# Kernel optimization log

Hardware: AMD Instinct MI355X
Metric: run time of the kernel (lower is better)

The kernel has to match this reference:

```python
import jax, jax.numpy as jnp
import numpy as np

NUM_HEADS = 8
MAX_REL = 32  # max_relative_positions
LN_EPS = 1e-5


def _conv1x1(x, W, b):
    # x: (B, C, H, W), W: (Cout, Cin), b: (Cout,)
    return jnp.einsum('bchw,oc->bohw', x, W) + b[None, :, None, None]


def setup_inputs() -> dict:
    key = jax.random.key(0)
    ks = jax.random.split(key, 10)
    B, C, H, W = 2, 512, 48, 48
    L = H * W
    s = 1.0 / np.sqrt(C)
    inp = {
        'x': jax.random.normal(ks[0], (B, C, H, W), jnp.float32),
        'mask': jax.random.randint(ks[1], (1, NUM_HEADS, L, L), 0, 2).astype(bool),
        'learnable_pos': jax.random.normal(ks[2], (1, C, H, W), jnp.float32) * 0.02,
        'Wq': jax.random.normal(ks[3], (C, C), jnp.float32) * s,
        'bq': jnp.zeros((C,), jnp.float32),
        'Wk': jax.random.normal(ks[4], (C, C), jnp.float32) * s,
        'bk': jnp.zeros((C,), jnp.float32),
        'Wv': jax.random.normal(ks[5], (C, C), jnp.float32) * s,
        'bv': jnp.zeros((C,), jnp.float32),
        'Wo': jax.random.normal(ks[6], (C, C), jnp.float32) * s,
        'bo': jnp.zeros((C,), jnp.float32),
        'rel_table': jax.random.normal(ks[7], (NUM_HEADS, 2 * MAX_REL + 1), jnp.float32) * 0.02,
        'ln_gamma': jnp.ones((C,), jnp.float32),
        'ln_beta': jnp.zeros((C,), jnp.float32),
    }
    return inp


def reference(x, mask, learnable_pos, Wq, bq, Wk, bk, Wv, bv, Wo, bo,
              rel_table, ln_gamma, ln_beta):
    B, C, H, W = x.shape
    L = H * W
    hd = C // NUM_HEADS
    residual = x

    xp = x + learnable_pos
    q = _conv1x1(xp, Wq, bq)
    k = _conv1x1(xp, Wk, bk)
    v = _conv1x1(xp, Wv, bv)

    def split_heads(t):  # (B,C,H,W) -> (B, heads, L, hd)
        return t.reshape(B, NUM_HEADS, hd, L).transpose(0, 1, 3, 2)

    q, k, v = split_heads(q), split_heads(k), split_heads(v)

    scale = 1.0 / np.sqrt(hd).astype(np.float32)
    scores = jnp.einsum('bhld,bhmd->bhlm', q, k) * scale  # (B,H,L,L)

    # relative positional bias per head
    pos = jnp.arange(L)
    rp = jnp.clip(pos[:, None] - pos[None, :], -MAX_REL, MAX_REL) + MAX_REL  # (L,L)
    scores = scores + rel_table[:, rp][None]  # (1,heads,L,L) broadcast

    scores = jnp.where(mask, scores, jnp.float32(-1e9))
    attn = jax.nn.softmax(scores, axis=-1)

    out = jnp.einsum('bhlm,bhmd->bhld', attn, v)  # (B,heads,L,hd)
    out = out.transpose(0, 1, 3, 2).reshape(B, C, H, W)
    out = _conv1x1(out, Wo, bo)

    y = residual + out
    # LayerNorm over channels (channels-last permute in original)
    yl = y.transpose(0, 2, 3, 1)  # (B,H,W,C)
    mu = jnp.mean(yl, axis=-1, keepdims=True)
    var = jnp.var(yl, axis=-1, keepdims=True)
    yl = (yl - mu) * jax.lax.rsqrt(var + LN_EPS) * ln_gamma + ln_beta
    return yl.transpose(0, 3, 1, 2)
```

## Files before the change

kernel.cpp:

```cpp
#include <hip/hip_runtime.h>
#include <cstdint>

#define L_SEQ 2304
#define CDIM  512
#define NHEADS 8
#define HD    64
#define LL    ((size_t)L_SEQ * L_SEQ)
#define ROWS_TOT (16 * L_SEQ)
#define PERBL ((size_t)2 * L_SEQ * 512)

typedef short  s8v  __attribute__((ext_vector_type(8)));
typedef float  f4v  __attribute__((ext_vector_type(4)));

__device__ __forceinline__ ushort f2bf(float f) {
    union { float f; uint32_t u; } v; v.f = f;
    uint32_t u = v.u;
    uint32_t r = (u + 0x7FFFu + ((u >> 16) & 1u)) >> 16;
    return (ushort)r;
}

__device__ __forceinline__ float bf2f(ushort u) {
    union { uint32_t u; float f; } v; v.u = (uint32_t)u << 16;
    return v.f;
}

__global__ __launch_bounds__(256) void prep_w(
    const float* __restrict__ Wq, const float* __restrict__ Wk,
    const float* __restrict__ Wv, const float* __restrict__ Wo,
    ushort* __restrict__ wf)
{
    const int i    = blockIdx.x * 256 + threadIdx.x;
    const int lane = i & 63;
    const int F    = (i >> 6) & 63;
    const int ob   = (i >> 12) & 7;
    const int mat  = i >> 15;
    const float* src = (mat == 0) ? Wq : (mat == 1) ? Wk : (mat == 2) ? Wv : Wo;
    const int row = ob * 64 + (F & 3) * 16 + (lane & 15);
    const int col = (F >> 2) * 32 + (lane >> 4) * 8;
    const float4 w0 = *(const float4*)&src[(size_t)row * 512 + col];
    const float4 w1 = *(const float4*)&src[(size_t)row * 512 + col + 4];
    ushort4 o0, o1;
    o0.x = f2bf(w0.x); o0.y = f2bf(w0.y); o0.z = f2bf(w0.z); o0.w = f2bf(w0.w);
    o1.x = f2bf(w1.x); o1.y = f2bf(w1.y); o1.z = f2bf(w1.z); o1.w = f2bf(w1.w);
    *(ushort4*)&wf[(size_t)i * 8]     = o0;
    *(ushort4*)&wf[(size_t)i * 8 + 4] = o1;
}

__global__ __launch_bounds__(256) void xpose(
    const float* __restrict__ x, const float* __restrict__ pos,
    ushort* __restrict__ xt)
{
    __shared__ ushort T[64][72];
    const int l0 = blockIdx.x * 64;
    const int c0 = blockIdx.y * 64;
    const int b  = blockIdx.z;
    const int t  = threadIdx.x;
    const int cc = t >> 2;
    const int l4 = (t & 3) * 16;
    const size_t off  = ((size_t)b * CDIM + c0 + cc) * L_SEQ + l0 + l4;
    const size_t poff = (size_t)(c0 + cc) * L_SEQ + l0 + l4;
    #pragma unroll
    for (int j4 = 0; j4 < 4; j4++) {
        const float4 xv = *(const float4*)&x[off + j4 * 4];
        const float4 pv = *(const float4*)&pos[poff + j4 * 4];
        T[cc][l4 + j4 * 4 + 0] = f2bf(xv.x + pv.x);
        T[cc][l4 + j4 * 4 + 1] = f2bf(xv.y + pv.y);
        T[cc][l4 + j4 * 4 + 2] = f2bf(xv.z + pv.z);
        T[cc][l4 + j4 * 4 + 3] = f2bf(xv.w + pv.w);
    }
    __syncthreads();
    const int lr = t >> 2;
    const int c4 = (t & 3) * 16;
    ushort o[16];
    #pragma unroll
    for (int j = 0; j < 16; j++) o[j] = T[c4 + j][lr];
    ushort* dst = &xt[((size_t)b * L_SEQ + l0 + lr) * 512 + c0 + c4];
    *(ushort4*)&dst[0]  = *(ushort4*)&o[0];
    *(ushort4*)&dst[4]  = *(ushort4*)&o[4];
    *(ushort4*)&dst[8]  = *(ushort4*)&o[8];
    *(ushort4*)&dst[12] = *(ushort4*)&o[12];
}

__global__ __launch_bounds__(256) void qkv_mfma(
    const ushort* __restrict__ xt, const ushort* __restrict__ wf,
    const float* __restrict__ bq, const float* __restrict__ bk,
    const float* __restrict__ bv,
    ushort* __restrict__ q_t, ushort* __restrict__ k_t, ushort* __restrict__ v_t)
{
    const int l0 = blockIdx.x * 64;
    const int ob = blockIdx.y;
    const int o0 = ob * 64;
    const int b  = blockIdx.z;
    const int t = threadIdx.x, w = t >> 6, lane = t & 63;
    const int n16 = lane & 15, q4 = lane >> 4;

    const ushort* A = xt + ((size_t)b * L_SEQ + l0 + w * 16 + n16) * 512 + q4 * 8;

    s8v areg[16];
    #pragma unroll
    for (int i = 0; i < 16; i++) areg[i] = *(const s8v*)&A[i * 32];

    const size_t lb = (size_t)lane * 8;

    f4v acc[3][4] = {};
    for (int ks = 0; ks < 16; ks++) {
        s8v bf[3][4];
        #pragma unroll
        for (int m = 0; m < 3; m++)
            #pragma unroll
            for (int t4 = 0; t4 < 4; t4++)
                bf[m][t4] = *(const s8v*)&wf[
                    ((size_t)((m * 8 + ob) * 64 + ks * 4 + t4)) * 512 + lb];
        const s8v a = areg[ks];
        #pragma unroll
        for (int m = 0; m < 3; m++)
            #pragma unroll
            for (int t4 = 0; t4 < 4; t4++)
                acc[m][t4] = __builtin_amdgcn_mfma_f32_16x16x32_bf16(a, bf[m][t4], acc[m][t4], 0, 0, 0);
    }

    const int h = ob;
    const int rowbase = l0 + w * 16 + q4 * 4;

    #pragma unroll
    for (int m = 0; m < 2; m++) {
        const float* bias = (m == 0) ? bq : bk;
        const float sc = (m == 0) ? 0.125f : 1.0f;
        ushort* op = (m == 0 ? q_t : k_t) + ((size_t)(b * NHEADS + h)) * L_SEQ * HD;
        #pragma unroll
        for (int t4 = 0; t4 < 4; t4++) {
            const float bi = bias[o0 + t4 * 16 + n16];
            #pragma unroll
            for (int r = 0; r < 4; r++)
                op[(size_t)(rowbase + r) * HD + t4 * 16 + n16] = f2bf((acc[m][t4][r] + bi) * sc);
        }
    }
    {
        ushort* op = v_t + ((size_t)(b * NHEADS + h)) * HD * L_SEQ;
        #pragma unroll
        for (int t4 = 0; t4 < 4; t4++) {
            const float bi = bv[o0 + t4 * 16 + n16];
            ushort4 st;
            st.x = f2bf(acc[2][t4][0] + bi);
            st.y = f2bf(acc[2][t4][1] + bi);
            st.z = f2bf(acc[2][t4][2] + bi);
            st.w = f2bf(acc[2][t4][3] + bi);
            *(ushort4*)&op[(size_t)(t4 * 16 + n16) * L_SEQ + rowbase] = st;
        }
    }
}

__global__ __launch_bounds__(256) void flash_attn_mfma(
    const ushort* __restrict__ q, const ushort* __restrict__ k,
    const ushort* __restrict__ vt, const int* __restrict__ mask,
    const float* __restrict__ rel_table, ushort* __restrict__ Opart,
    float* __restrict__ Lpart)
{
    __shared__ __align__(16) ushort Kf[512 * 8];
    __shared__ __align__(16) ushort Vf[512 * 8];
    __shared__ __align__(16) ushort Pb[4 * 16 * 72];
    __shared__ float rt[65];

    const int t    = threadIdx.x;
    const int id   = blockIdx.x;
    const int h    = id & 7;
    const int s2   = id >> 3;
    const int b    = s2 & 1;
    const int half = (s2 >> 1) & 1;
    const int qb   = s2 >> 2;
    const int bh   = b * NHEADS + h;
    const int l0   = qb * 64;
    const int w    = t >> 6;
    const int lane = t & 63;
    const int n16  = lane & 15;
    const int q4   = lane >> 4;

    if (t < 65) rt[t] = rel_table[h * 65 + t];

    const ushort* qp = q  + (size_t)bh * L_SEQ * HD;
    const ushort* kp = k  + (size_t)bh * L_SEQ * HD;
    const ushort* vp = vt + (size_t)bh * HD * L_SEQ;
    const int*    mp = mask + (size_t)h * LL;

    const int qrow = l0 + w * 16 + n16;
    const s8v qA0 = *(const s8v*)&qp[(size_t)qrow * HD + q4 * 8];
    const s8v qA1 = *(const s8v*)&qp[(size_t)qrow * HD + 32 + q4 * 8];

    f4v O[4] = {{0.f,0.f,0.f,0.f},{0.f,0.f,0.f,0.f},{0.f,0.f,0.f,0.f},{0.f,0.f,0.f,0.f}};
    float lrun[4] = {0.f, 0.f, 0.f, 0.f};

    int sKey[2], sD0[2], sDd[2];
    #pragma unroll
    for (int cc = 0; cc < 2; cc++) {
        const int c = t + cc * 256;
        const int g = c >> 6;
        const int sT = g >> 1, sS = g & 1;
        const int sQ = (c >> 4) & 3, sN = c & 15;
        sKey[cc] = sT * 16 + sN;
        sD0[cc]  = sS * 32 + sQ * 8;
        sDd[cc]  = sT * 16 + sN;
    }

    const int rowbase = l0 + w * 16 + q4 * 4;
    const int kbase = half * 1152;

    s8v kreg[2], vreg[2];
    int mreg[4][4];
    #pragma unroll
    for (int cc = 0; cc < 2; cc++) {
        kreg[cc] = *(const s8v*)&kp[(size_t)(kbase + sKey[cc]) * HD + sD0[cc]];
        vreg[cc] = *(const s8v*)&vp[(size_t)sDd[cc] * L_SEQ + kbase + sD0[cc]];
    }
    #pragma unroll
    for (int t4 = 0; t4 < 4; t4++)
        #pragma unroll
        for (int r = 0; r < 4; r++)
            mreg[t4][r] = mp[(size_t)(rowbase + r) * L_SEQ + kbase + t4 * 16 + n16];

    for (int mt = 0; mt < 18; mt++) {
        const int mb = kbase + mt * 64;
        __syncthreads();
        #pragma unroll
        for (int cc = 0; cc < 2; cc++) {
            const int c = t + cc * 256;
            *(s8v*)&Kf[c * 8] = kreg[cc];
            *(s8v*)&Vf[c * 8] = vreg[cc];
        }
        __syncthreads();

        const int mb2 = (mt < 17) ? mb + 64 : mb;
        s8v knx[2], vnx[2];
        int mnx[4][4];
        #pragma unroll
        for (int cc = 0; cc < 2; cc++) {
            knx[cc] = *(const s8v*)&kp[(size_t)(mb2 + sKey[cc]) * HD + sD0[cc]];
            vnx[cc] = *(const s8v*)&vp[(size_t)sDd[cc] * L_SEQ + mb2 + sD0[cc]];
        }
        #pragma unroll
        for (int t4 = 0; t4 < 4; t4++)
            #pragma unroll
            for (int r = 0; r < 4; r++)
                mnx[t4][r] = mp[(size_t)(rowbase + r) * L_SEQ + mb2 + t4 * 16 + n16];

        f4v S[4];
        #pragma unroll
        for (int t4 = 0; t4 < 4; t4++) {
            const s8v b0 = *(const s8v*)&Kf[((t4 * 2 + 0) * 64 + lane) * 8];
            const s8v b1 = *(const s8v*)&Kf[((t4 * 2 + 1) * 64 + lane) * 8];
            f4v acc = {0.f, 0.f, 0.f, 0.f};
            acc = __builtin_amdgcn_mfma_f32_16x16x32_bf16(qA0, b0, acc, 0, 0, 0);
            acc = __builtin_amdgcn_mfma_f32_16x16x32_bf16(qA1, b1, acc, 0, 0, 0);
            S[t4] = acc;
        }

        #pragma unroll
        for (int t4 = 0; t4 < 4; t4++) {
            const int A = (l0 + w * 16) - (mb + t4 * 16);
            if (A >= 47) {
                const float bu = rt[64];
                #pragma unroll
                for (int r = 0; r < 4; r++) S[t4][r] += bu;
            } else if (A <= -47) {
                const float bu = rt[0];
                #pragma unroll
                for (int r = 0; r < 4; r++) S[t4][r] += bu;
            } else {
                #pragma unroll
                for (int r = 0; r < 4; r++) {
                    int dix = A + q4 * 4 + r - n16;
                    dix = min(max(dix, -32), 32) + 32;
                    S[t4][r] += rt[dix];
                }
            }
            #pragma unroll
            for (int r = 0; r < 4; r++)
                if (mreg[t4][r] == 0) S[t4][r] = -1e9f;
        }

        float sum[4] = {0.f, 0.f, 0.f, 0.f};
        #pragma unroll
        for (int r = 0; r < 4; r++) {
            #pragma unroll
            for (int t4 = 0; t4 < 4; t4++) {
                const float p = __expf(S[t4][r]);
                sum[r] += p;
                Pb[w * 1152 + (q4 * 4 + r) * 72 + t4 * 16 + n16] = f2bf(p);
            }
        }

        const s8v pf0 = *(const s8v*)&Pb[w * 1152 + n16 * 72 + q4 * 8];
        const s8v pf1 = *(const s8v*)&Pb[w * 1152 + n16 * 72 + 32 + q4 * 8];
        #pragma unroll
        for (int t4 = 0; t4 < 4; t4++) {
            f4v o = O[t4];
            const s8v v0 = *(const s8v*)&Vf[((t4 * 2 + 0) * 64 + lane) * 8];
            const s8v v1 = *(const s8v*)&Vf[((t4 * 2 + 1) * 64 + lane) * 8];
            o = __builtin_amdgcn_mfma_f32_16x16x32_bf16(pf0, v0, o, 0, 0, 0);
            o = __builtin_amdgcn_mfma_f32_16x16x32_bf16(pf1, v1, o, 0, 0, 0);
            O[t4] = o;
        }

        #pragma unroll
        for (int r = 0; r < 4; r++) {
            float s = sum[r];
            s += __shfl_xor(s, 1);
            s += __shfl_xor(s, 2);
            s += __shfl_xor(s, 4);
            s += __shfl_xor(s, 8);
            lrun[r] += s;
        }

        #pragma unroll
        for (int cc = 0; cc < 2; cc++) { kreg[cc] = knx[cc]; vreg[cc] = vnx[cc]; }
        #pragma unroll
        for (int t4 = 0; t4 < 4; t4++)
            #pragma unroll
            for (int r = 0; r < 4; r++)
                mreg[t4][r] = mnx[t4][r];
    }

    ushort* op = Opart + (size_t)half * PERBL + (size_t)b * L_SEQ * 512;
    #pragma unroll
    for (int r = 0; r < 4; r++) {
        const size_t base = (size_t)(rowbase + r) * 512 + h * 64;
        #pragma unroll
        for (int t4 = 0; t4 < 4; t4++)
            op[base + t4 * 16 + n16] = f2bf(O[t4][r]);
    }
    if (n16 == 0) {
        const size_t sb = (size_t)half * ROWS_TOT + (size_t)bh * L_SEQ;
        #pragma unroll
        for (int r = 0; r < 4; r++)
            Lpart[sb + rowbase + r] = lrun[r];
    }
}

__global__ __launch_bounds__(256) void combine_kernel(
    const ushort* __restrict__ O01, const float* __restrict__ Lp,
    ushort* __restrict__ at)
{
    const int i   = blockIdx.x * 256 + threadIdx.x;
    const int c8  = i & 63;
    const int row = i >> 6;
    const int b   = row / L_SEQ;
    const int l   = row - b * L_SEQ;
    const int h   = c8 >> 3;
    const size_t s = (size_t)(b * NHEADS + h) * L_SEQ + l;
    const float f = 1.0f / (Lp[s] + Lp[ROWS_TOT + s]);
    const size_t o = (size_t)row * 512 + c8 * 8;
    const ushort4 a0 = *(const ushort4*)&O01[o];
    const ushort4 a1 = *(const ushort4*)&O01[o + 4];
    const ushort4 c0 = *(const ushort4*)&O01[PERBL + o];
    const ushort4 c1 = *(const ushort4*)&O01[PERBL + o + 4];
    ushort4 r0, r1;
    r0.x = f2bf((bf2f(a0.x) + bf2f(c0.x)) * f);
    r0.y = f2bf((bf2f(a0.y) + bf2f(c0.y)) * f);
    r0.z = f2bf((bf2f(a0.z) + bf2f(c0.z)) * f);
    r0.w = f2bf((bf2f(a0.w) + bf2f(c0.w)) * f);
    r1.x = f2bf((bf2f(a1.x) + bf2f(c1.x)) * f);
    r1.y = f2bf((bf2f(a1.y) + bf2f(c1.y)) * f);
    r1.z = f2bf((bf2f(a1.z) + bf2f(c1.z)) * f);
    r1.w = f2bf((bf2f(a1.w) + bf2f(c1.w)) * f);
    *(ushort4*)&at[o]     = r0;
    *(ushort4*)&at[o + 4] = r1;
}

__global__ __launch_bounds__(256) void out_mfma(
    const ushort* __restrict__ at, const ushort* __restrict__ wf,
    const float* __restrict__ bo, const float* __restrict__ x,
    float* __restrict__ y)
{
    const int l0 = blockIdx.x * 64;
    const int ob = blockIdx.y;
    const int o0 = ob * 64;
    const int b  = blockIdx.z;
    const int t = threadIdx.x, w = t >> 6, lane = t & 63;
    const int n16 = lane & 15, q4 = lane >> 4;

    const ushort* A = at + ((size_t)b * L_SEQ + l0 + w * 16 + n16) * 512 + q4 * 8;

    s8v areg[16];
    #pragma unroll
    for (int i = 0; i < 16; i++) areg[i] = *(const s8v*)&A[i * 32];

    const size_t lb = (size_t)lane * 8;

    f4v acc[4] = {{0.f,0.f,0.f,0.f},{0.f,0.f,0.f,0.f},{0.f,0.f,0.f,0.f},{0.f,0.f,0.f,0.f}};
    for (int ks = 0; ks < 16; ks++) {
        s8v bf[4];
        #pragma unroll
        for (int t4 = 0; t4 < 4; t4++)
            bf[t4] = *(const s8v*)&wf[
                ((size_t)((3 * 8 + ob) * 64 + ks * 4 + t4)) * 512 + lb];
        const s8v a = areg[ks];
        #pragma unroll
        for (int t4 = 0; t4 < 4; t4++)
            acc[t4] = __builtin_amdgcn_mfma_f32_16x16x32_bf16(a, bf[t4], acc[t4], 0, 0, 0);
    }

    const int rowbase = l0 + w * 16 + q4 * 4;
    #pragma unroll
    for (int t4 = 0; t4 < 4; t4++) {
        const int o = o0 + t4 * 16 + n16;
        const float bi = bo[o];
        const size_t off = ((size_t)b * CDIM + o) * L_SEQ + rowbase;
        const float4 xv = *(const float4*)&x[off];
        float4 st;
        st.x = acc[t4][0] + bi + xv.x;
        st.y = acc[t4][1] + bi + xv.y;
        st.z = acc[t4][2] + bi + xv.z;
        st.w = acc[t4][3] + bi + xv.w;
        *(float4*)&y[off] = st;
    }
}

__global__ __launch_bounds__(256) void ln_kernel(
    float* __restrict__ y, const float* __restrict__ gamma,
    const float* __restrict__ beta)
{
    const int t = threadIdx.x;
    const int p = t & 31;
    const int g = t >> 5;
    const int pos = blockIdx.x * 32 + p;
    const int b = (pos >= L_SEQ) ? 1 : 0;
    const int l = pos - b * L_SEQ;
    float* col = y + (size_t)b * CDIM * L_SEQ + l;

    float s = 0.f, sq = 0.f;
    for (int c = g * 64; c < g * 64 + 64; c++) {
        const float v = col[(size_t)c * L_SEQ];
        s += v; sq += v * v;
    }
    __shared__ float S1[8][32];
    __shared__ float S2[8][32];
    S1[g][p] = s; S2[g][p] = sq;
    __syncthreads();
    if (t < 32) {
        float ss = 0.f, qq = 0.f;
        #pragma unroll
        for (int gg = 0; gg < 8; gg++) { ss += S1[gg][t]; qq += S2[gg][t]; }
        const float mu = ss * (1.0f / CDIM);
        const float var = qq * (1.0f / CDIM) - mu * mu;
        S1[0][t] = mu;
        S2[0][t] = rsqrtf(var + 1e-5f);
    }
    __syncthreads();
    const float mu = S1[0][p];
    const float rs = S2[0][p];
    for (int c = g * 64; c < g * 64 + 64; c++) {
        const float v = col[(size_t)c * L_SEQ];
        col[(size_t)c * L_SEQ] = (v - mu) * rs * gamma[c] + beta[c];
    }
}

extern "C" void kernel_launch(void* const* d_in, const int* in_sizes, int n_in,
                              void* d_out, int out_size, void* d_ws, size_t ws_size,
                              hipStream_t stream) {
    const float* x    = (const float*)d_in[0];
    const int* mask   = (const int*)d_in[1];
    const float* pos  = (const float*)d_in[2];
    const float* Wq   = (const float*)d_in[3];
    const float* bq   = (const float*)d_in[4];
    const float* Wk   = (const float*)d_in[5];
    const float* bk   = (const float*)d_in[6];
    const float* Wv   = (const float*)d_in[7];
    const float* bv   = (const float*)d_in[8];
    const float* Wo   = (const float*)d_in[9];
    const float* bo   = (const float*)d_in[10];
    const float* rel  = (const float*)d_in[11];
    const float* gam  = (const float*)d_in[12];
    const float* bet  = (const float*)d_in[13];

    ushort* qw  = (ushort*)d_ws;
    ushort* kw  = qw + PERBL;
    ushort* vw  = kw + PERBL;
    ushort* xtw = vw + PERBL;
    ushort* wbw = xtw + PERBL;
    ushort* Opart = wbw + (size_t)4 * 262144;
    float* Lpart = (float*)(Opart + 2 * PERBL);
    ushort* attnT = xtw;
    float* y = (float*)d_out;

    prep_w<<<dim3(512), 256, 0, stream>>>(Wq, Wk, Wv, Wo, wbw);

    xpose<<<dim3(L_SEQ / 64, CDIM / 64, 2), 256, 0, stream>>>(x, pos, xtw);

    qkv_mfma<<<dim3(L_SEQ / 64, CDIM / 64, 2), 256, 0, stream>>>(
        xtw, wbw, bq, bk, bv, qw, kw, vw);

    flash_attn_mfma<<<dim3(1152), 256, 0, stream>>>(qw, kw, vw, mask, rel,
                                                    Opart, Lpart);

    combine_kernel<<<dim3(1152), 256, 0, stream>>>(Opart, Lpart, attnT);

    out_mfma<<<dim3(L_SEQ / 64, CDIM / 64, 2), 256, 0, stream>>>(
        attnT, wbw, bo, x, y);

    ln_kernel<<<(2 * L_SEQ) / 32, 256, 0, stream>>>(y, gam, bet);
}
```

Before: 366.6 us.

## Fuse prep kernels, fold split-K combine into output GEMM, double-buffer K/V LDS

Merges weight conversion and input transpose into one launch, removes the separate combine kernel by normalizing and summing the two partial attention outputs while loading A-fragments in the output projection, and double-buffers K/V tiles in shared memory in the flash attention loop to drop one barrier per iteration. This cuts kernel launches and an intermediate round-trip through memory. In exchange the output GEMM reads twice as much partial data per block (repeated across output-channel blocks), and the extra LDS may lower attention occupancy.

```diff
diff --git a/kernel.cpp b/kernel.cpp
--- a/kernel.cpp
+++ b/kernel.cpp
@@ -24,61 +24,61 @@
     return v.f;
 }
 
-__global__ __launch_bounds__(256) void prep_w(
+__global__ __launch_bounds__(256) void prep(
     const float* __restrict__ Wq, const float* __restrict__ Wk,
     const float* __restrict__ Wv, const float* __restrict__ Wo,
-    ushort* __restrict__ wf)
-{
-    const int i    = blockIdx.x * 256 + threadIdx.x;
-    const int lane = i & 63;
-    const int F    = (i >> 6) & 63;
-    const int ob   = (i >> 12) & 7;
-    const int mat  = i >> 15;
-    const float* src = (mat == 0) ? Wq : (mat == 1) ? Wk : (mat == 2) ? Wv : Wo;
-    const int row = ob * 64 + (F & 3) * 16 + (lane & 15);
-    const int col = (F >> 2) * 32 + (lane >> 4) * 8;
-    const float4 w0 = *(const float4*)&src[(size_t)row * 512 + col];
-    const float4 w1 = *(const float4*)&src[(size_t)row * 512 + col + 4];
-    ushort4 o0, o1;
-    o0.x = f2bf(w0.x); o0.y = f2bf(w0.y); o0.z = f2bf(w0.z); o0.w = f2bf(w0.w);
-    o1.x = f2bf(w1.x); o1.y = f2bf(w1.y); o1.z = f2bf(w1.z); o1.w = f2bf(w1.w);
-    *(ushort4*)&wf[(size_t)i * 8]     = o0;
-    *(ushort4*)&wf[(size_t)i * 8 + 4] = o1;
-}
-
-__global__ __launch_bounds__(256) void xpose(
     const float* __restrict__ x, const float* __restrict__ pos,
-    ushort* __restrict__ xt)
+    ushort* __restrict__ wf, ushort* __restrict__ xt)
 {
     __shared__ ushort T[64][72];
-    const int l0 = blockIdx.x * 64;
-    const int c0 = blockIdx.y * 64;
-    const int b  = blockIdx.z;
+    const int bx = blockIdx.x;
     const int t  = threadIdx.x;
-    const int cc = t >> 2;
-    const int l4 = (t & 3) * 16;
-    const size_t off  = ((size_t)b * CDIM + c0 + cc) * L_SEQ + l0 + l4;
-    const size_t poff = (size_t)(c0 + cc) * L_SEQ + l0 + l4;
-    #pragma unroll
-    for (int j4 = 0; j4 < 4; j4++) {
-        const float4 xv = *(const float4*)&x[off + j4 * 4];
-        const float4 pv = *(const float4*)&pos[poff + j4 * 4];
-        T[cc][l4 + j4 * 4 + 0] = f2bf(xv.x + pv.x);
-        T[cc][l4 + j4 * 4 + 1] = f2bf(xv.y + pv.y);
-        T[cc][l4 + j4 * 4 + 2] = f2bf(xv.z + pv.z);
-        T[cc][l4 + j4 * 4 + 3] = f2bf(xv.w + pv.w);
-    }
-    __syncthreads();
-    const int lr = t >> 2;
-    const int c4 = (t & 3) * 16;
-    ushort o[16];
-    #pragma unroll
-    for (int j = 0; j < 16; j++) o[j] = T[c4 + j][lr];
-    ushort* dst = &xt[((size_t)b * L_SEQ + l0 + lr) * 512 + c0 + c4];
-    *(ushort4*)&dst[0]  = *(ushort4*)&o[0];
-    *(ushort4*)&dst[4]  = *(ushort4*)&o[4];
-    *(ushort4*)&dst[8]  = *(ushort4*)&o[8];
-    *(ushort4*)&dst[12] = *(ushort4*)&o[12];
+    if (bx < 512) {
+        const int i    = bx * 256 + t;
+        const int lane = i & 63;
+        const int F    = (i >> 6) & 63;
+        const int ob   = (i >> 12) & 7;
+        const int mat  = i >> 15;
+        const float* src = (mat == 0) ? Wq : (mat == 1) ? Wk : (mat == 2) ? Wv : Wo;
+        const int row = ob * 64 + (F & 3) * 16 + (lane & 15);
+        const int col = (F >> 2) * 32 + (lane >> 4) * 8;
+        const float4 w0 = *(const float4*)&src[(size_t)row * 512 + col];
+        const float4 w1 = *(const float4*)&src[(size_t)row * 512 + col + 4];
+        ushort4 o0, o1;
+        o0.x = f2bf(w0.x); o0.y = f2bf(w0.y); o0.z = f2bf(w0.z); o0.w = f2bf(w0.w);
+        o1.x = f2bf(w1.x); o1.y = f2bf(w1.y); o1.z = f2bf(w1.z); o1.w = f2bf(w1.w);
+        *(ushort4*)&wf[(size_t)i * 8]     = o0;
+        *(ushort4*)&wf[(size_t)i * 8 + 4] = o1;
+    } else {
+        const int bb = bx - 512;
+        const int l0 = (bb % 36) * 64;
+        const int c0 = ((bb / 36) & 7) * 64;
+        const int b  = bb / 288;
+        const int cc = t >> 2;
+        const int l4 = (t & 3) * 16;
+        const size_t off  = ((size_t)b * CDIM + c0 + cc) * L_SEQ + l0 + l4;
+        const size_t poff = (size_t)(c0 + cc) * L_SEQ + l0 + l4;
+        #pragma unroll
+        for (int j4 = 0; j4 < 4; j4++) {
+            const float4 xv = *(const float4*)&x[off + j4 * 4];
+            const float4 pv = *(const float4*)&pos[poff + j4 * 4];
+            T[cc][l4 + j4 * 4 + 0] = f2bf(xv.x + pv.x);
+            T[cc][l4 + j4 * 4 + 1] = f2bf(xv.y + pv.y);
+            T[cc][l4 + j4 * 4 + 2] = f2bf(xv.z + pv.z);
+            T[cc][l4 + j4 * 4 + 3] = f2bf(xv.w + pv.w);
+        }
+        __syncthreads();
+        const int lr = t >> 2;
+        const int c4 = (t & 3) * 16;
+        ushort o[16];
+        #pragma unroll
+        for (int j = 0; j < 16; j++) o[j] = T[c4 + j][lr];
+        ushort* dst = &xt[((size_t)b * L_SEQ + l0 + lr) * 512 + c0 + c4];
+        *(ushort4*)&dst[0]  = *(ushort4*)&o[0];
+        *(ushort4*)&dst[4]  = *(ushort4*)&o[4];
+        *(ushort4*)&dst[8]  = *(ushort4*)&o[8];
+        *(ushort4*)&dst[12] = *(ushort4*)&o[12];
+    }
 }
 
 __global__ __launch_bounds__(256) void qkv_mfma(
@@ -156,8 +156,8 @@
     const float* __restrict__ rel_table, ushort* __restrict__ Opart,
     float* __restrict__ Lpart)
 {
-    __shared__ __align__(16) ushort Kf[512 * 8];
-    __shared__ __align__(16) ushort Vf[512 * 8];
+    __shared__ __align__(16) ushort Kf[2][512 * 8];
+    __shared__ __align__(16) ushort Vf[2][512 * 8];
     __shared__ __align__(16) ushort Pb[4 * 16 * 72];
     __shared__ float rt[65];
 
@@ -217,14 +217,16 @@
         for (int r = 0; r < 4; r++)
             mreg[t4][r] = mp[(size_t)(rowbase + r) * L_SEQ + kbase + t4 * 16 + n16];
 
+    int par = 0;
     for (int mt = 0; mt < 18; mt++) {
         const int mb = kbase + mt * 64;
-        __syncthreads();
+        ushort* Kb = &Kf[par][0];
+        ushort* Vb = &Vf[par][0];
         #pragma unroll
         for (int cc = 0; cc < 2; cc++) {
             const int c = t + cc * 256;
-            *(s8v*)&Kf[c * 8] = kreg[cc];
-            *(s8v*)&Vf[c * 8] = vreg[cc];
+            *(s8v*)&Kb[c * 8] = kreg[cc];
+            *(s8v*)&Vb[c * 8] = vreg[cc];
         }
         __syncthreads();
 
@@ -245,8 +247,8 @@
         f4v S[4];
         #pragma unroll
         for (int t4 = 0; t4 < 4; t4++) {
-            const s8v b0 = *(const s8v*)&Kf[((t4 * 2 + 0) * 64 + lane) * 8];
-            const s8v b1 = *(const s8v*)&Kf[((t4 * 2 + 1) * 64 + lane) * 8];
+            const s8v b0 = *(const s8v*)&Kb[((t4 * 2 + 0) * 64 + lane) * 8];
+            const s8v b1 = *(const s8v*)&Kb[((t4 * 2 + 1) * 64 + lane) * 8];
             f4v acc = {0.f, 0.f, 0.f, 0.f};
             acc = __builtin_amdgcn_mfma_f32_16x16x32_bf16(qA0, b0, acc, 0, 0, 0);
             acc = __builtin_amdgcn_mfma_f32_16x16x32_bf16(qA1, b1, acc, 0, 0, 0);
@@ -293,8 +295,8 @@
         #pragma unroll
         for (int t4 = 0; t4 < 4; t4++) {
             f4v o = O[t4];
-            const s8v v0 = *(const s8v*)&Vf[((t4 * 2 + 0) * 64 + lane) * 8];
-            const s8v v1 = *(const s8v*)&Vf[((t4 * 2 + 1) * 64 + lane) * 8];
+            const s8v v0 = *(const s8v*)&Vb[((t4 * 2 + 0) * 64 + lane) * 8];
+            const s8v v1 = *(const s8v*)&Vb[((t4 * 2 + 1) * 64 + lane) * 8];
             o = __builtin_amdgcn_mfma_f32_16x16x32_bf16(pf0, v0, o, 0, 0, 0);
             o = __builtin_amdgcn_mfma_f32_16x16x32_bf16(pf1, v1, o, 0, 0, 0);
             O[t4] = o;
@@ -317,6 +319,7 @@
             #pragma unroll
             for (int r = 0; r < 4; r++)
                 mreg[t4][r] = mnx[t4][r];
+        par ^= 1;
     }
 
     ushort* op = Opart + (size_t)half * PERBL + (size_t)b * L_SEQ * 512;
@@ -335,40 +338,10 @@
     }
 }
 
-__global__ __launch_bounds__(256) void combine_kernel(
-    const ushort* __restrict__ O01, const float* __restrict__ Lp,
-    ushort* __restrict__ at)
-{
-    const int i   = blockIdx.x * 256 + threadIdx.x;
-    const int c8  = i & 63;
-    const int row = i >> 6;
-    const int b   = row / L_SEQ;
-    const int l   = row - b * L_SEQ;
-    const int h   = c8 >> 3;
-    const size_t s = (size_t)(b * NHEADS + h) * L_SEQ + l;
-    const float f = 1.0f / (Lp[s] + Lp[ROWS_TOT + s]);
-    const size_t o = (size_t)row * 512 + c8 * 8;
-    const ushort4 a0 = *(const ushort4*)&O01[o];
-    const ushort4 a1 = *(const ushort4*)&O01[o + 4];
-    const ushort4 c0 = *(const ushort4*)&O01[PERBL + o];
-    const ushort4 c1 = *(const ushort4*)&O01[PERBL + o + 4];
-    ushort4 r0, r1;
-    r0.x = f2bf((bf2f(a0.x) + bf2f(c0.x)) * f);
-    r0.y = f2bf((bf2f(a0.y) + bf2f(c0.y)) * f);
-    r0.z = f2bf((bf2f(a0.z) + bf2f(c0.z)) * f);
-    r0.w = f2bf((bf2f(a0.w) + bf2f(c0.w)) * f);
-    r1.x = f2bf((bf2f(a1.x) + bf2f(c1.x)) * f);
-    r1.y = f2bf((bf2f(a1.y) + bf2f(c1.y)) * f);
-    r1.z = f2bf((bf2f(a1.z) + bf2f(c1.z)) * f);
-    r1.w = f2bf((bf2f(a1.w) + bf2f(c1.w)) * f);
-    *(ushort4*)&at[o]     = r0;
-    *(ushort4*)&at[o + 4] = r1;
-}
-
 __global__ __launch_bounds__(256) void out_mfma(
-    const ushort* __restrict__ at, const ushort* __restrict__ wf,
-    const float* __restrict__ bo, const float* __restrict__ x,
-    float* __restrict__ y)
+    const ushort* __restrict__ Opart, const float* __restrict__ Lp,
+    const ushort* __restrict__ wf, const float* __restrict__ bo,
+    const float* __restrict__ x, float* __restrict__ y)
 {
     const int l0 = blockIdx.x * 64;
     const int ob = blockIdx.y;
@@ -377,11 +350,37 @@
     const int t = threadIdx.x, w = t >> 6, lane = t & 63;
     const int n16 = lane & 15, q4 = lane >> 4;
 
-    const ushort* A = at + ((size_t)b * L_SEQ + l0 + w * 16 + n16) * 512 + q4 * 8;
+    const int l = l0 + w * 16 + n16;
+
+    float fsc[8];
+    #pragma unroll
+    for (int h = 0; h < 8; h++) {
+        const size_t s = (size_t)(b * NHEADS + h) * L_SEQ + l;
+        fsc[h] = 1.0f / (Lp[s] + Lp[ROWS_TOT + s]);
+    }
+
+    const ushort* o0p = Opart + ((size_t)b * L_SEQ + l) * 512 + q4 * 8;
+    const ushort* o1p = o0p + PERBL;
 
     s8v areg[16];
     #pragma unroll
-    for (int i = 0; i < 16; i++) areg[i] = *(const s8v*)&A[i * 32];
+    for (int ks = 0; ks < 16; ks++) {
+        const ushort4 a0 = *(const ushort4*)&o0p[ks * 32];
+        const ushort4 a1 = *(const ushort4*)&o0p[ks * 32 + 4];
+        const ushort4 c0 = *(const ushort4*)&o1p[ks * 32];
+        const ushort4 c1 = *(const ushort4*)&o1p[ks * 32 + 4];
+        const float f = fsc[ks >> 1];
+        s8v a;
+        a[0] = (short)f2bf((bf2f(a0.x) + bf2f(c0.x)) * f);
+        a[1] = (short)f2bf((bf2f(a0.y) + bf2f(c0.y)) * f);
+        a[2] = (short)f2bf((bf2f(a0.z) + bf2f(c0.z)) * f);
+        a[3] = (short)f2bf((bf2f(a0.w) + bf2f(c0.w)) * f);
+        a[4] = (short)f2bf((bf2f(a1.x) + bf2f(c1.x)) * f);
+        a[5] = (short)f2bf((bf2f(a1.y) + bf2f(c1.y)) * f);
+        a[6] = (short)f2bf((bf2f(a1.z) + bf2f(c1.z)) * f);
+        a[7] = (short)f2bf((bf2f(a1.w) + bf2f(c1.w)) * f);
+        areg[ks] = a;
+    }
 
     const size_t lb = (size_t)lane * 8;
 
@@ -478,12 +477,9 @@
     ushort* wbw = xtw + PERBL;
     ushort* Opart = wbw + (size_t)4 * 262144;
     float* Lpart = (float*)(Opart + 2 * PERBL);
-    ushort* attnT = xtw;
     float* y = (float*)d_out;
 
-    prep_w<<<dim3(512), 256, 0, stream>>>(Wq, Wk, Wv, Wo, wbw);
-
-    xpose<<<dim3(L_SEQ / 64, CDIM / 64, 2), 256, 0, stream>>>(x, pos, xtw);
+    prep<<<dim3(512 + 576), 256, 0, stream>>>(Wq, Wk, Wv, Wo, x, pos, wbw, xtw);
 
     qkv_mfma<<<dim3(L_SEQ / 64, CDIM / 64, 2), 256, 0, stream>>>(
         xtw, wbw, bq, bk, bv, qw, kw, vw);
@@ -491,10 +487,8 @@
     flash_attn_mfma<<<dim3(1152), 256, 0, stream>>>(qw, kw, vw, mask, rel,
                                                     Opart, Lpart);
 
-    combine_kernel<<<dim3(1152), 256, 0, stream>>>(Opart, Lpart, attnT);
-
     out_mfma<<<dim3(L_SEQ / 64, CDIM / 64, 2), 256, 0, stream>>>(
-        attnT, wbw, bo, x, y);
+        Opart, Lpart, wbw, bo, x, y);
 
     ln_kernel<<<(2 * L_SEQ) / 32, 256, 0, stream>>>(y, gam, bet);
 }
```

Result: no change. 366.0 us (-0.2%).
